# Performance work log

Measured on AMD Instinct MI355X. Metric: run time of the kernel, lower is better.

## Reference

```python
import jax, jax.numpy as jnp
import numpy as np

T = 4
SCALE = 5.0  # triangle surrogate scale (unused in pure forward)


def setup_inputs() -> dict:
    key = jax.random.key(0)
    k1, _ = jax.random.split(key)
    # [T*B, C, H, W]; uniform [0,4) so membrane (init 4.0) crosses thresh=8 within T steps
    x = jax.random.uniform(k1, (256, 128, 32, 32), dtype=jnp.float32) * 4.0
    thresh = jnp.ones((1,), dtype=jnp.float32) * 8.0
    return {"x": x, "thresh": thresh}


def reference(x, thresh):
    # expand: [T*B, C, H, W] -> [T, B, C, H, W]
    xs = x.reshape((T, x.shape[0] // T) + x.shape[1:])
    mem0 = jnp.broadcast_to(0.5 * thresh, xs.shape[1:]).astype(x.dtype)

    def step(mem, xt):
        mem = mem + xt
        spike_bin = (mem >= thresh).astype(mem.dtype)  # IF threshold compare
        spike = spike_bin * thresh
        mem = mem - spike  # hard reset by subtraction
        return mem, spike

    _, spikes = jax.lax.scan(step, mem0, xs)  # spikes: [T, B, C, H, W]
    # merge: flatten(0,1) -> [T*B, C, H, W]
    return spikes.reshape(x.shape)
```

## Files before the change

kernel.cpp:

```cpp
#include <hip/hip_runtime.h>


__global__ __launch_bounds__(256) void if_fwd_kernel(
    const float4* __restrict__ x,
    const float* __restrict__ thresh_p,
    float4* __restrict__ out,
    int n4)
{
    const float th = thresh_p[0];
    const float m0 = 0.5f * th;

    const int stride = gridDim.x * blockDim.x;
    for (int i = blockIdx.x * blockDim.x + threadIdx.x; i < n4; i += stride) {
        float4 v0 = x[0 * n4 + i];
        float4 v1 = x[1 * n4 + i];
        float4 v2 = x[2 * n4 + i];
        float4 v3 = x[3 * n4 + i];

        float4 m = make_float4(m0, m0, m0, m0);

        float4 s;
        m.x += v0.x; m.y += v0.y; m.z += v0.z; m.w += v0.w;
        s.x = (m.x >= th) ? th : 0.0f;
        s.y = (m.y >= th) ? th : 0.0f;
        s.z = (m.z >= th) ? th : 0.0f;
        s.w = (m.w >= th) ? th : 0.0f;
        out[0 * n4 + i] = s;
        m.x -= s.x; m.y -= s.y; m.z -= s.z; m.w -= s.w;
        m.x += v1.x; m.y += v1.y; m.z += v1.z; m.w += v1.w;
        s.x = (m.x >= th) ? th : 0.0f;
        s.y = (m.y >= th) ? th : 0.0f;
        s.z = (m.z >= th) ? th : 0.0f;
        s.w = (m.w >= th) ? th : 0.0f;
        out[1 * n4 + i] = s;
        m.x -= s.x; m.y -= s.y; m.z -= s.z; m.w -= s.w;
        m.x += v2.x; m.y += v2.y; m.z += v2.z; m.w += v2.w;
        s.x = (m.x >= th) ? th : 0.0f;
        s.y = (m.y >= th) ? th : 0.0f;
        s.z = (m.z >= th) ? th : 0.0f;
        s.w = (m.w >= th) ? th : 0.0f;
        out[2 * n4 + i] = s;
        m.x -= s.x; m.y -= s.y; m.z -= s.z; m.w -= s.w;
        m.x += v3.x; m.y += v3.y; m.z += v3.z; m.w += v3.w;
        s.x = (m.x >= th) ? th : 0.0f;
        s.y = (m.y >= th) ? th : 0.0f;
        s.z = (m.z >= th) ? th : 0.0f;
        s.w = (m.w >= th) ? th : 0.0f;
        out[3 * n4 + i] = s;
    }
}

extern "C" void kernel_launch(void* const* d_in, const int* in_sizes, int n_in,
                              void* d_out, int out_size, void* d_ws, size_t ws_size,
                              hipStream_t stream) {
    const float* x      = (const float*)d_in[0];
    const float* thresh = (const float*)d_in[1];
    float* out          = (float*)d_out;

    const int total   = in_sizes[0];
    const int n_per_t = total / 4;
    const int n4      = n_per_t / 4;

    const int block = 256;
    int grid = (n4 + block - 1) / block;
    if (grid > 2048) grid = 2048;

    if_fwd_kernel<<<grid, block, 0, stream>>>(
        (const float4*)x, thresh, (float4*)out, n4);
}
```

Baseline: 238.6 us.

## Assign contiguous chunks per block with 512-thread blocks and native vector type

Replaces the grid-stride loop with 256 blocks of 512 threads, each covering one contiguous chunk of the per-timestep array, and switches to clang ext_vector float4 arithmetic. The goal is better DRAM locality per block and fewer scheduling overheads. With only 256 blocks on a GPU with 256 CUs, each CU holds a single block, which may lower occupancy and memory-level parallelism. The code also assumes n4 divides evenly by the grid, leaving any remainder unprocessed for other shapes.

```diff
diff --git a/kernel.cpp b/kernel.cpp
--- a/kernel.cpp
+++ b/kernel.cpp
@@ -1,47 +1,55 @@
 #include <hip/hip_runtime.h>
 
 
-__global__ __launch_bounds__(256) void if_fwd_kernel(
-    const float4* __restrict__ x,
+typedef float f32x4 __attribute__((ext_vector_type(4)));
+
+__global__ __launch_bounds__(512) void if_fwd_kernel(
+    const f32x4* __restrict__ x,
     const float* __restrict__ thresh_p,
-    float4* __restrict__ out,
-    int n4)
+    f32x4* __restrict__ out,
+    int n4,
+    int chunk)
 {
     const float th = thresh_p[0];
     const float m0 = 0.5f * th;
 
-    const int stride = gridDim.x * blockDim.x;
-    for (int i = blockIdx.x * blockDim.x + threadIdx.x; i < n4; i += stride) {
-        float4 v0 = x[0 * n4 + i];
-        float4 v1 = x[1 * n4 + i];
-        float4 v2 = x[2 * n4 + i];
-        float4 v3 = x[3 * n4 + i];
+    const int begin = blockIdx.x * chunk;
+    const int end   = begin + chunk;
 
-        float4 m = make_float4(m0, m0, m0, m0);
+    for (int i = begin + threadIdx.x; i < end; i += 512) {
+        f32x4 v0 = x[0 * n4 + i];
+        f32x4 v1 = x[1 * n4 + i];
+        f32x4 v2 = x[2 * n4 + i];
+        f32x4 v3 = x[3 * n4 + i];
 
-        float4 s;
-        m.x += v0.x; m.y += v0.y; m.z += v0.z; m.w += v0.w;
+        f32x4 m = m0;
+        f32x4 s;
+
+        m += v0;
         s.x = (m.x >= th) ? th : 0.0f;
         s.y = (m.y >= th) ? th : 0.0f;
         s.z = (m.z >= th) ? th : 0.0f;
         s.w = (m.w >= th) ? th : 0.0f;
         out[0 * n4 + i] = s;
-        m.x -= s.x; m.y -= s.y; m.z -= s.z; m.w -= s.w;
-        m.x += v1.x; m.y += v1.y; m.z += v1.z; m.w += v1.w;
+        m -= s;
+
+        m += v1;
         s.x = (m.x >= th) ? th : 0.0f;
         s.y = (m.y >= th) ? th : 0.0f;
         s.z = (m.z >= th) ? th : 0.0f;
         s.w = (m.w >= th) ? th : 0.0f;
         out[1 * n4 + i] = s;
-        m.x -= s.x; m.y -= s.y; m.z -= s.z; m.w -= s.w;
-        m.x += v2.x; m.y += v2.y; m.z += v2.z; m.w += v2.w;
+        m -= s;
+
+        m += v2;
         s.x = (m.x >= th) ? th : 0.0f;
         s.y = (m.y >= th) ? th : 0.0f;
         s.z = (m.z >= th) ? th : 0.0f;
         s.w = (m.w >= th) ? th : 0.0f;
         out[2 * n4 + i] = s;
-        m.x -= s.x; m.y -= s.y; m.z -= s.z; m.w -= s.w;
-        m.x += v3.x; m.y += v3.y; m.z += v3.z; m.w += v3.w;
+        m -= s;
+
+        m += v3;
         s.x = (m.x >= th) ? th : 0.0f;
         s.y = (m.y >= th) ? th : 0.0f;
         s.z = (m.z >= th) ? th : 0.0f;
@@ -61,10 +69,10 @@
     const int n_per_t = total / 4;
     const int n4      = n_per_t / 4;
 
-    const int block = 256;
-    int grid = (n4 + block - 1) / block;
-    if (grid > 2048) grid = 2048;
+    const int block = 512;
+    const int grid  = 256;
+    const int chunk = n4 / grid;
 
     if_fwd_kernel<<<grid, block, 0, stream>>>(
-        (const float4*)x, thresh, (float4*)out, n4);
+        (const f32x4*)x, thresh, (f32x4*)out, n4, chunk);
 }
```

New measurement: 237.6 us. No clear change (-0.4%).
